# Optimization experiments

Hardware: AMD Instinct MI355X
Metric: run time of the kernel (lower is better)

Reference implementation:

```python
import jax, jax.numpy as jnp
import numpy as np

K = 8          # number of TR cores / modes
D = 1024       # categories per mode
R = 64         # TR rank
NDRAWS = 2048
EPS = 1e-30


def setup_inputs() -> dict:
    key = jax.random.key(0)
    ks = jax.random.split(key, K)
    inp = {f"log_core{i}": jax.random.normal(ks[i], (D, R, R), dtype=jnp.float32)
           for i in range(K)}
    inp["n_draws"] = NDRAWS
    return inp


def _sample(cores, n_draws, seed=1):
    """Batched version of trip_index_sample: all draws sampled in parallel."""
    k = len(cores)
    # heads[j] = S_0 @ ... @ S_{j-1} with S_i = core_i.sum(0); heads[0] = None
    heads = [None]
    acc = cores[0].sum(axis=0)
    for c in cores[1:]:
        heads.append(acc)
        acc = acc @ c.sum(axis=0)
    norm = acc  # S_0 ... S_{K-1}

    keys = jax.random.split(jax.random.key(seed), k)
    tail = None          # [B, r_{j+1}, r_K] running suffix product per draw
    idxs = []
    for step, j in enumerate(range(k - 1, -1, -1)):
        core, head = cores[j], heads[j]
        if tail is None:
            # first step (j = K-1): marginal weights shared by all draws
            if head is None:  # degenerate K == 1 case
                w = jnp.trace(core, axis1=1, axis2=2)
            else:
                w = jnp.einsum('ab,nba->n', head, core)
            ix = jax.random.categorical(keys[step], jnp.log(jnp.clip(w, EPS)),
                                        shape=(n_draws,))
            tail = core[ix]  # [B, r_j, r_K]
        else:
            # M = tail @ head : [B, r_{j+1}, r_j] (head is None only at j == 0,
            # where r_0 == r_K so tail already has the right shape)
            M = tail if head is None else tail @ head
            w = jnp.einsum('nab,Bba->Bn', core, M)  # [B, d_j]
            ix = jax.random.categorical(keys[step], jnp.log(jnp.clip(w, EPS)),
                                        axis=-1)
            tail = jnp.einsum('Bab,Bbc->Bac', core[ix], tail)
        idxs.append(ix)
    sample = jnp.stack(idxs[::-1], axis=1)  # [B, K], mode order 0..K-1
    log_p = jnp.log(jnp.clip(jnp.trace(tail, axis1=1, axis2=2), EPS)) \
            - jnp.log(jnp.trace(norm))
    return sample, log_p


def reference(log_core0, log_core1, log_core2, log_core3,
              log_core4, log_core5, log_core6, log_core7, n_draws):
    log_cores = [log_core0, log_core1, log_core2, log_core3,
                 log_core4, log_core5, log_core6, log_core7]
    cores = [jax.nn.softplus(c) for c in log_cores]
    sample, log_p = _sample(cores, n_draws)
    return sample, log_p
```

## Files before the change

kernel.cpp:

```cpp
#include <hip/hip_runtime.h>
#include <stdint.h>
#include <math.h>

#define D_CAT  1024
#define R_TR   64
#define RR     4096
#define NDRAWS 2048
#define KMODES 8

struct CorePtrs { const float* p[KMODES]; };

typedef __attribute__((ext_vector_type(8))) __bf16 bf16x8;
typedef __attribute__((ext_vector_type(4))) float  f32x4;
typedef unsigned int u32;

union BF8 { ushort u[8]; bf16x8 v; };

static __device__ inline void async_cp16(const void* g, void* l) {
  __builtin_amdgcn_global_load_lds(
      (const __attribute__((address_space(1))) u32*)g,
      (__attribute__((address_space(3))) u32*)l, 16, 0, 0);
}

static __host__ __device__ inline uint32_t rotl32(uint32_t x, int r) {
  return (x << r) | (x >> (32 - r));
}
static __host__ __device__ inline void tf2x32(uint32_t k1, uint32_t k2,
                                              uint32_t x0, uint32_t x1,
                                              uint32_t& o0, uint32_t& o1) {
  uint32_t ks0 = k1, ks1 = k2, ks2 = k1 ^ k2 ^ 0x1BD11BDAu;
  x0 += ks0; x1 += ks1;
  x0 += x1; x1 = rotl32(x1, 13); x1 ^= x0;
  x0 += x1; x1 = rotl32(x1, 15); x1 ^= x0;
  x0 += x1; x1 = rotl32(x1, 26); x1 ^= x0;
  x0 += x1; x1 = rotl32(x1, 6);  x1 ^= x0;
  x0 += ks1; x1 += ks2 + 1u;
  x0 += x1; x1 = rotl32(x1, 17); x1 ^= x0;
  x0 += x1; x1 = rotl32(x1, 29); x1 ^= x0;
  x0 += x1; x1 = rotl32(x1, 16); x1 ^= x0;
  x0 += x1; x1 = rotl32(x1, 24); x1 ^= x0;
  x0 += ks2; x1 += ks0 + 2u;
  x0 += x1; x1 = rotl32(x1, 13); x1 ^= x0;
  x0 += x1; x1 = rotl32(x1, 15); x1 ^= x0;
  x0 += x1; x1 = rotl32(x1, 26); x1 ^= x0;
  x0 += x1; x1 = rotl32(x1, 6);  x1 ^= x0;
  x0 += ks0; x1 += ks1 + 3u;
  x0 += x1; x1 = rotl32(x1, 17); x1 ^= x0;
  x0 += x1; x1 = rotl32(x1, 29); x1 ^= x0;
  x0 += x1; x1 = rotl32(x1, 16); x1 ^= x0;
  x0 += x1; x1 = rotl32(x1, 24); x1 ^= x0;
  x0 += ks1; x1 += ks2 + 4u;
  x0 += x1; x1 = rotl32(x1, 13); x1 ^= x0;
  x0 += x1; x1 = rotl32(x1, 15); x1 ^= x0;
  x0 += x1; x1 = rotl32(x1, 26); x1 ^= x0;
  x0 += x1; x1 = rotl32(x1, 6);  x1 ^= x0;
  x0 += ks2; x1 += ks0 + 5u;
  o0 = x0; o1 = x1;
}

static __device__ inline float softplus_fast(float x) {
  float e = __expf(-fabsf(x));
  return fmaxf(x, 0.0f) + __logf(1.0f + e);
}

static __device__ inline unsigned short f32_bf16(float f) {
  uint32_t u = __float_as_uint(f);
  u += 0x7fffu + ((u >> 16) & 1u);
  return (unsigned short)(u >> 16);
}

static __device__ inline float gumbel_at(uint32_t k1, uint32_t k2, uint32_t e) {
  uint32_t o0, o1;
  tf2x32(k1, k2, 0u, e, o0, o1);
  uint32_t bits = o0 ^ o1;
  float f = __uint_as_float((bits >> 9) | 0x3F800000u) - 1.0f;
  float u = (f > 0.0f) ? f : 1.17549435e-38f;
  return -logf(-logf(u));
}


__global__ void k_sentinel(float* out, int n) {
  int i = blockIdx.x * 256 + threadIdx.x;
  if (i < n) out[i] = -12288.0f;
}

__global__ __launch_bounds__(256) void k_spart(CorePtrs cp, float* __restrict__ Spart) {
  const int bid = blockIdx.x, tid = threadIdx.x;
  const int i = bid >> 8, c = bid & 255;
  const float* src = cp.p[i] + (size_t)c * 4 * RR;
  float acc[16];
#pragma unroll
  for (int k = 0; k < 16; ++k) acc[k] = 0.0f;
#pragma unroll
  for (int d = 0; d < 4; ++d) {
    const float* row = src + (size_t)d * RR;
#pragma unroll
    for (int k = 0; k < 16; ++k)
      acc[k] += softplus_fast(row[tid + k * 256]);
  }
  float* dst = Spart + (size_t)bid * RR;
#pragma unroll
  for (int k = 0; k < 16; ++k) dst[tid + k * 256] = acc[k];
}

__global__ __launch_bounds__(256) void k_sreduce(const float* __restrict__ Spart,
                                                 double* __restrict__ S) {
  const int idx = blockIdx.x * 256 + threadIdx.x;
  const int i = idx >> 12, rr = idx & 4095;
  const float* p = Spart + ((size_t)i << 20) + rr;
  double a0 = 0.0, a1 = 0.0, a2 = 0.0, a3 = 0.0;
  for (int c = 0; c < 256; c += 4) {
    a0 += (double)p[(size_t)(c + 0) * RR];
    a1 += (double)p[(size_t)(c + 1) * RR];
    a2 += (double)p[(size_t)(c + 2) * RR];
    a3 += (double)p[(size_t)(c + 3) * RR];
  }
  S[idx] = (a0 + a1) + (a2 + a3);
}

__global__ __launch_bounds__(256) void k_heads(const double* __restrict__ S,
                                               double* __restrict__ heads,
                                               double* __restrict__ misc) {
  __shared__ double cur[RR];
  __shared__ double Sm[RR];
  __shared__ double tbuf[64];
  const int tid = threadIdx.x;
  const int bcol = tid & 63;
  const int a0 = tid >> 6;
#pragma unroll
  for (int k = 0; k < 16; ++k) {
    int p = tid + k * 256;
    double v = S[p];
    cur[p] = v;
    heads[p] = v;
  }
  __syncthreads();
  for (int m = 1; m <= 6; ++m) {
#pragma unroll
    for (int k = 0; k < 16; ++k) {
      int p = tid + k * 256;
      Sm[p] = S[(size_t)m * RR + p];
    }
    __syncthreads();
    double acc[16];
#pragma unroll
    for (int k = 0; k < 16; ++k) acc[k] = 0.0;
    for (int c = 0; c < 64; ++c) {
      double s = Sm[c * 64 + bcol];
#pragma unroll
      for (int k = 0; k < 16; ++k)
        acc[k] = fma(cur[(a0 + 4 * k) * 64 + c], s, acc[k]);
    }
    __syncthreads();
#pragma unroll
    for (int k = 0; k < 16; ++k) {
      int p = tid + k * 256;
      cur[p] = acc[k];
      heads[(size_t)m * RR + p] = acc[k];
    }
    __syncthreads();
  }
#pragma unroll
  for (int k = 0; k < 16; ++k) {
    int p = tid + k * 256;
    Sm[p] = S[(size_t)7 * RR + p];
  }
  __syncthreads();
  if (tid < 64) {
    double acc = 0.0;
    for (int c = 0; c < 64; ++c)
      acc = fma(cur[tid * 64 + c], Sm[c * 64 + tid], acc);
    tbuf[tid] = acc;
  }
  __syncthreads();
  if (tid == 0) {
    double tr = 0.0;
    for (int a = 0; a < 64; ++a) tr += tbuf[a];
    misc[0] = log(tr);
  }
}

__global__ __launch_bounds__(256) void k_softplus(const float* __restrict__ src,
                                                  ushort* __restrict__ Bh,
                                                  ushort* __restrict__ Bl) {
  const size_t i4 = ((size_t)blockIdx.x * 256 + threadIdx.x) * 4;
  float4 v = *(const float4*)(src + i4);
  const float ov[4] = {softplus_fast(v.x), softplus_fast(v.y),
                       softplus_fast(v.z), softplus_fast(v.w)};
  ushort h4[4], l4[4];
#pragma unroll
  for (int q = 0; q < 4; ++q) {
    ushort h = f32_bf16(ov[q]);
    float hf = __uint_as_float((uint32_t)h << 16);
    h4[q] = h;
    l4[q] = f32_bf16(ov[q] - hf);
  }
  *(ushort4*)(Bh + i4) = make_ushort4(h4[0], h4[1], h4[2], h4[3]);
  *(ushort4*)(Bl + i4) = make_ushort4(l4[0], l4[1], l4[2], l4[3]);
}

__global__ __launch_bounds__(256) void k_w0(const float* __restrict__ raw,
                                            const double* __restrict__ head7,
                                            float* __restrict__ W) {
  const int tid = threadIdx.x;
  const int lane = tid & 63;
  const int n = blockIdx.x * 4 + (tid >> 6);
  const float* crow = raw + (size_t)n * RR;
  double acc = 0.0;
  for (int q = lane; q < RR; q += 64)
    acc = fma((double)softplus_fast(crow[q]), head7[(q & 63) * 64 + (q >> 6)], acc);
  for (int m = 32; m; m >>= 1) acc += __shfl_xor(acc, m);
  if (lane == 0) W[n] = (float)acc;
}

__global__ __launch_bounds__(256) void k_mt2(const float* __restrict__ tail,
                                             const double* __restrict__ head, int useHead,
                                             ushort* __restrict__ Ah,
                                             ushort* __restrict__ Al) {
  __shared__ alignas(16) ushort hT[2][4096];
  const int tid = threadIdx.x;
#pragma unroll
  for (int rep = 0; rep < 16; ++rep) {
    int i = tid + rep * 256;
    float v;
    if (useHead) v = (float)head[(i & 63) * 64 + (i >> 6)];
    else         v = ((i >> 6) == (i & 63)) ? 1.0f : 0.0f;
    ushort h = f32_bf16(v);
    float hf = __uint_as_float((uint32_t)h << 16);
    int dst = (i & 0xFC0) | (((((i >> 3) & 7) ^ ((i >> 6) & 7)) << 3)) | (i & 7);
    hT[0][dst] = h;
    hT[1][dst] = f32_bf16(v - hf);
  }
  __syncthreads();

  const int w = tid >> 6, l = tid & 63;
  const int B = blockIdx.x * 4 + w;
  const float* tb = tail + (size_t)B * RR;
  const int lrow = l & 15, kg = l >> 4;

  ushort* ah_out = Ah + (size_t)B * RR;
  ushort* al_out = Al + (size_t)B * RR;

  for (int it = 0; it < 4; ++it) {
    BF8 afh[2], afl[2];
#pragma unroll
    for (int kt = 0; kt < 2; ++kt) {
      const float* src = tb + (it * 16 + lrow) * 64 + kt * 32 + kg * 8;
      float4 v0 = *(const float4*)src;
      float4 v1 = *(const float4*)(src + 4);
      float vv[8] = {v0.x, v0.y, v0.z, v0.w, v1.x, v1.y, v1.z, v1.w};
#pragma unroll
      for (int q = 0; q < 8; ++q) {
        ushort h = f32_bf16(vv[q]);
        float hf = __uint_as_float((uint32_t)h << 16);
        afh[kt].u[q] = h;
        afl[kt].u[q] = f32_bf16(vv[q] - hf);
      }
    }
#pragma unroll
    for (int kt2 = 0; kt2 < 4; ++kt2) {
      f32x4 hh = (f32x4)0.0f, sm = (f32x4)0.0f;
#pragma unroll
      for (int kt = 0; kt < 2; ++kt) {
        int rowB = kt2 * 16 + lrow;
        int kcA  = kt * 4 + kg;
        int off  = rowB * 64 + ((kcA ^ (rowB & 7)) << 3);
        bf16x8 bh = *(const bf16x8*)&hT[0][off];
        bf16x8 bl = *(const bf16x8*)&hT[1][off];
        hh = __builtin_amdgcn_mfma_f32_16x16x32_bf16(afh[kt].v, bh, hh, 0, 0, 0);
        sm = __builtin_amdgcn_mfma_f32_16x16x32_bf16(afh[kt].v, bl, sm, 0, 0, 0);
        sm = __builtin_amdgcn_mfma_f32_16x16x32_bf16(afl[kt].v, bh, sm, 0, 0, 0);
      }
      ushort h4[4], l4[4];
#pragma unroll
      for (int q = 0; q < 4; ++q) {
        float v = hh[q] + sm[q];
        ushort h = f32_bf16(v);
        float hf = __uint_as_float((uint32_t)h << 16);
        h4[q] = h;
        l4[q] = f32_bf16(v - hf);
      }
      int o = (kt2 * 16 + lrow) * 64 + it * 16 + kg * 4;
      *(ushort4*)(ah_out + o) = make_ushort4(h4[0], h4[1], h4[2], h4[3]);
      *(ushort4*)(al_out + o) = make_ushort4(l4[0], l4[1], l4[2], l4[3]);
    }
  }
}

__global__ __launch_bounds__(256) void k_wgemm(const ushort* __restrict__ Ah,
                                               const ushort* __restrict__ Al,
                                               const ushort* __restrict__ Bh,
                                               const ushort* __restrict__ Bl,
                                               float* __restrict__ W) {
  __shared__ ushort lds[2][4 * 4096];
  const int tid = threadIdx.x;
  const int L = blockIdx.x;
  const int x = L & 7, j = L >> 3;
  const int bn = (x & 1) * 8 + (j & 7);
  const int bb = (x >> 1) * 8 + (j >> 3);
  const int w = tid >> 6, l = tid & 63;

  const int srow = l >> 3;
  const int skc  = l & 7;
  const ushort* gbase;
  {
    const ushort* bases[4] = {Ah + (size_t)bb * 64 * RR, Al + (size_t)bb * 64 * RR,
                              Bh + (size_t)bn * 64 * RR, Bl + (size_t)bn * 64 * RR};
    gbase = bases[w] + (size_t)srow * RR + (size_t)((skc ^ srow) * 8);
  }

  const int wm = (w >> 1) * 32, wn = (w & 1) * 32;
  const int lrow = l & 15;
  const int kg   = l >> 4;

  f32x4 acc_hh[2][2], acc_sm[2][2], hht[2][2];
#pragma unroll
  for (int mt = 0; mt < 2; ++mt)
#pragma unroll
    for (int nt = 0; nt < 2; ++nt) {
      acc_hh[mt][nt] = (f32x4)0.0f;
      acc_sm[mt][nt] = (f32x4)0.0f;
      hht[mt][nt]    = (f32x4)0.0f;
    }

  int roffA[2][2], roffB[2][2];
#pragma unroll
  for (int mt = 0; mt < 2; ++mt)
#pragma unroll
    for (int kt = 0; kt < 2; ++kt) {
      int rowA = wm + mt * 16 + lrow;
      int kcA  = kt * 4 + kg;
      roffA[mt][kt] = rowA * 64 + ((kcA ^ (rowA & 7)) << 3);
      int rowB = wn + mt * 16 + lrow;
      roffB[mt][kt] = rowB * 64 + ((kcA ^ (rowB & 7)) << 3);
    }

#pragma unroll
  for (int q = 0; q < 8; ++q)
    async_cp16(gbase + (size_t)q * 8 * RR, &lds[0][w * 4096 + q * 512]);

  for (int t = 0; t < 64; ++t) {
    const int bf = t & 1;
    __syncthreads();
    if (t < 63) {
      const int koff = (t + 1) * 64;
#pragma unroll
      for (int q = 0; q < 8; ++q)
        async_cp16(gbase + (size_t)q * 8 * RR + koff,
                   &lds[bf ^ 1][w * 4096 + q * 512]);
    }
    const ushort* L2 = lds[bf];
#pragma unroll
    for (int kt = 0; kt < 2; ++kt) {
      bf16x8 ah[2], al[2], bh[2], bl[2];
#pragma unroll
      for (int mt = 0; mt < 2; ++mt) {
        ah[mt] = *(const bf16x8*)&L2[0 * 4096 + roffA[mt][kt]];
        al[mt] = *(const bf16x8*)&L2[1 * 4096 + roffA[mt][kt]];
      }
#pragma unroll
      for (int nt = 0; nt < 2; ++nt) {
        bh[nt] = *(const bf16x8*)&L2[2 * 4096 + roffB[nt][kt]];
        bl[nt] = *(const bf16x8*)&L2[3 * 4096 + roffB[nt][kt]];
      }
#pragma unroll
      for (int mt = 0; mt < 2; ++mt)
#pragma unroll
        for (int nt = 0; nt < 2; ++nt) {
          acc_hh[mt][nt] = __builtin_amdgcn_mfma_f32_16x16x32_bf16(ah[mt], bh[nt], acc_hh[mt][nt], 0, 0, 0);
          acc_sm[mt][nt] = __builtin_amdgcn_mfma_f32_16x16x32_bf16(ah[mt], bl[nt], acc_sm[mt][nt], 0, 0, 0);
          acc_sm[mt][nt] = __builtin_amdgcn_mfma_f32_16x16x32_bf16(al[mt], bh[nt], acc_sm[mt][nt], 0, 0, 0);
        }
    }
    if ((t & 15) == 15) {
#pragma unroll
      for (int mt = 0; mt < 2; ++mt)
#pragma unroll
        for (int nt = 0; nt < 2; ++nt) {
          hht[mt][nt] += acc_hh[mt][nt];
          acc_hh[mt][nt] = (f32x4)0.0f;
        }
    }
  }

#pragma unroll
  for (int mt = 0; mt < 2; ++mt)
#pragma unroll
    for (int nt = 0; nt < 2; ++nt)
#pragma unroll
      for (int q = 0; q < 4; ++q) {
        int gr = bb * 64 + wm + mt * 16 + kg * 4 + q;
        int gc = bn * 64 + wn + nt * 16 + lrow;
        W[(size_t)gr * D_CAT + gc] = hht[mt][nt][q] + acc_sm[mt][nt][q];
      }
}

__global__ __launch_bounds__(256) void k_sample(const float* __restrict__ W, int shared_row,
                                                uint32_t key1, uint32_t key2,
                                                int* __restrict__ ixout,
                                                float* __restrict__ out, int mode_j) {
  const int b = blockIdx.x, tid = threadIdx.x;
  const float* wrow = W + (shared_row ? 0 : (size_t)b * D_CAT);
  float best = -3.4e38f; int bidx = 0x7fffffff;
  for (int k = 0; k < 4; ++k) {
    int n = tid + k * 256;
    float lg = logf(fmaxf(wrow[n], 1e-30f));
    float v = gumbel_at(key1, key2, (uint32_t)(b * D_CAT + n)) + lg;
    if (v > best || (v == best && n < bidx)) { best = v; bidx = n; }
  }
  for (int m = 32; m; m >>= 1) {
    float ov = __shfl_xor(best, m);
    int   oi = __shfl_xor(bidx, m);
    if (ov > best || (ov == best && oi < bidx)) { best = ov; bidx = oi; }
  }
  __shared__ float sv[4];
  __shared__ int   si[4];
  if ((tid & 63) == 0) { sv[tid >> 6] = best; si[tid >> 6] = bidx; }
  __syncthreads();
  if (tid == 0) {
    for (int t = 1; t < 4; ++t)
      if (sv[t] > best || (sv[t] == best && si[t] < bidx)) { best = sv[t]; bidx = si[t]; }
    ixout[b] = bidx;
    out[b * KMODES + mode_j] = (float)bidx;
  }
}

__global__ __launch_bounds__(256) void k_tail2(const float* __restrict__ raw,
                                               const ushort* __restrict__ Bh,
                                               const ushort* __restrict__ Bl,
                                               const int* __restrict__ ix,
                                               float* __restrict__ tail, int first) {
  const int B = blockIdx.x;
  const int tid = threadIdx.x;
  const int m = ix[B];
  float* trow = tail + (size_t)B * RR;
  if (first) {
    const float* crow = raw + (size_t)m * RR;
#pragma unroll
    for (int r = 0; r < 4; ++r) {
      float4 v = *(const float4*)(crow + tid * 4 + r * 1024);
      float4 o;
      o.x = softplus_fast(v.x); o.y = softplus_fast(v.y);
      o.z = softplus_fast(v.z); o.w = softplus_fast(v.w);
      *(float4*)(trow + tid * 4 + r * 1024) = o;
    }
    return;
  }
  __shared__ alignas(16) ushort Th[4096];
  __shared__ alignas(16) ushort Tl[4096];
  const ushort* ch = Bh + (size_t)m * RR;
  const ushort* cl = Bl + (size_t)m * RR;

#pragma unroll
  for (int r = 0; r < 4; ++r) {
    int p = tid * 4 + r * 1024;
    int i = p >> 6, k = p & 63;
    float4 v = *(const float4*)(trow + p);
    float vv[4] = {v.x, v.y, v.z, v.w};
#pragma unroll
    for (int q = 0; q < 4; ++q) {
      int row = k + q;
      int dst = row * 64 + ((((i >> 3) ^ (row & 7)) << 3)) + (i & 7);
      ushort h = f32_bf16(vv[q]);
      float hf = __uint_as_float((uint32_t)h << 16);
      Th[dst] = h;
      Tl[dst] = f32_bf16(vv[q] - hf);
    }
  }
  __syncthreads();

  const int w = tid >> 6, l = tid & 63;
  const int lrow = l & 15, kg = l >> 4;
  bf16x8 ah[2], al[2];
#pragma unroll
  for (int kt = 0; kt < 2; ++kt) {
    int off = (w * 16 + lrow) * 64 + kt * 32 + kg * 8;
    ah[kt] = *(const bf16x8*)(ch + off);
    al[kt] = *(const bf16x8*)(cl + off);
  }
#pragma unroll
  for (int jt = 0; jt < 4; ++jt) {
    f32x4 hh = (f32x4)0.0f, sm = (f32x4)0.0f;
#pragma unroll
    for (int kt = 0; kt < 2; ++kt) {
      int rowB = jt * 16 + lrow;
      int kcA  = kt * 4 + kg;
      int off  = rowB * 64 + ((kcA ^ (rowB & 7)) << 3);
      bf16x8 bh = *(const bf16x8*)&Th[off];
      bf16x8 bl = *(const bf16x8*)&Tl[off];
      hh = __builtin_amdgcn_mfma_f32_16x16x32_bf16(ah[kt], bh, hh, 0, 0, 0);
      sm = __builtin_amdgcn_mfma_f32_16x16x32_bf16(ah[kt], bl, sm, 0, 0, 0);
      sm = __builtin_amdgcn_mfma_f32_16x16x32_bf16(al[kt], bh, sm, 0, 0, 0);
      sm = __builtin_amdgcn_mfma_f32_16x16x32_bf16(al[kt], bl, sm, 0, 0, 0);
    }
#pragma unroll
    for (int q = 0; q < 4; ++q)
      trow[(w * 16 + kg * 4 + q) * 64 + jt * 16 + lrow] = hh[q] + sm[q];
  }
}

__global__ __launch_bounds__(256) void k_logp(const float* __restrict__ tail,
                                              const double* __restrict__ misc,
                                              float* __restrict__ out) {
  const int b = blockIdx.x * 256 + threadIdx.x;
  double tr = 0.0;
  for (int a = 0; a < 64; ++a) tr += (double)tail[(size_t)b * RR + a * 65];
  double lp = log(fmax(tr, 1e-30)) - misc[0];
  out[NDRAWS * KMODES + b] = (float)lp;
}

extern "C" void kernel_launch(void* const* d_in, const int* in_sizes, int n_in,
                              void* d_out, int out_size, void* d_ws, size_t ws_size,
                              hipStream_t stream) {
  (void)in_sizes; (void)n_in;
  CorePtrs cp;
  for (int i = 0; i < KMODES; ++i) cp.p[i] = (const float*)d_in[i];
  float* outf = (float*)d_out;

  char* base = (char*)d_ws;
  const size_t o_w     = 0;
  const size_t o_tail  = o_w + (size_t)NDRAWS * D_CAT * 4;
  const size_t o_ahl   = o_tail + (size_t)NDRAWS * RR * 4;
  const size_t o_spart = o_ahl;
  const size_t o_S     = o_ahl + (size_t)NDRAWS * RR * 4;
  const size_t o_heads = o_S + (size_t)KMODES * RR * 8;
  const size_t o_ix    = o_heads + (size_t)7 * RR * 8;
  const size_t o_misc  = o_ix + (size_t)NDRAWS * 4;
  const size_t o_bh    = o_misc + 256;
  const size_t o_bl    = o_bh + (size_t)D_CAT * RR * 2;
  const size_t NEED    = o_bl + (size_t)D_CAT * RR * 2;
  if (ws_size < NEED) {
    k_sentinel<<<(out_size + 255) / 256, 256, 0, stream>>>(outf, out_size);
    return;
  }

  float*  W     = (float*)(base + o_w);
  float*  tail  = (float*)(base + o_tail);
  ushort* Ah    = (ushort*)(base + o_ahl);
  ushort* Al    = Ah + (size_t)NDRAWS * RR;
  float*  Spart = (float*)(base + o_spart);
  double* S     = (double*)(base + o_S);
  double* heads = (double*)(base + o_heads);
  int*    ix    = (int*)(base + o_ix);
  double* misc  = (double*)(base + o_misc);
  ushort* Bh    = (ushort*)(base + o_bh);
  ushort* Bl    = (ushort*)(base + o_bl);

  uint32_t kk1[KMODES], kk2[KMODES];
  for (uint32_t s = 0; s < KMODES; ++s) tf2x32(0u, 1u, 0u, s, kk1[s], kk2[s]);

  k_spart  <<<2048, 256, 0, stream>>>(cp, Spart);
  k_sreduce<<<128,  256, 0, stream>>>(Spart, S);
  k_heads  <<<1,    256, 0, stream>>>(S, heads, misc);

  for (int s = 0; s < KMODES; ++s) {
    const int j = 7 - s;
    if (s == 0) {
      k_w0<<<256, 256, 0, stream>>>(cp.p[7], heads + (size_t)6 * RR, W);
    } else {
      k_softplus<<<4096, 256, 0, stream>>>(cp.p[j], Bh, Bl);
      k_mt2<<<512, 256, 0, stream>>>(tail, j > 0 ? heads + (size_t)(j - 1) * RR : nullptr,
                                     j > 0 ? 1 : 0, Ah, Al);
      k_wgemm<<<512, 256, 0, stream>>>(Ah, Al, Bh, Bl, W);
    }
    k_sample<<<NDRAWS, 256, 0, stream>>>(W, s == 0 ? 1 : 0, kk1[s], kk2[s], ix, outf, j);
    k_tail2 <<<2048, 256, 0, stream>>>(cp.p[j], Bh, Bl, ix, tail, s == 0 ? 1 : 0);
  }
  k_logp<<<KMODES, 256, 0, stream>>>(tail, misc, outf);
}
```

Measured before the change: 905.9 us.

## Fuse softplus with tail-head product and sampling with tail update kernels

Merges the per-mode softplus/bf16 split and the tail@head transform into one launch, with block ranges selecting the role. Merges categorical sampling with the tail update so the sampled index stays in shared memory instead of going through a global ix buffer. For the last mode (no head), replaces the identity-matrix MFMA product with a plain LDS transpose and bf16 split. This removes several kernel launches per mode and some redundant work. The cost is larger shared memory per block in the fused sampling kernel, which may lower occupancy.

```diff
diff --git a/kernel.cpp b/kernel.cpp
--- a/kernel.cpp
+++ b/kernel.cpp
@@ -180,25 +180,6 @@
   }
 }
 
-__global__ __launch_bounds__(256) void k_softplus(const float* __restrict__ src,
-                                                  ushort* __restrict__ Bh,
-                                                  ushort* __restrict__ Bl) {
-  const size_t i4 = ((size_t)blockIdx.x * 256 + threadIdx.x) * 4;
-  float4 v = *(const float4*)(src + i4);
-  const float ov[4] = {softplus_fast(v.x), softplus_fast(v.y),
-                       softplus_fast(v.z), softplus_fast(v.w)};
-  ushort h4[4], l4[4];
-#pragma unroll
-  for (int q = 0; q < 4; ++q) {
-    ushort h = f32_bf16(ov[q]);
-    float hf = __uint_as_float((uint32_t)h << 16);
-    h4[q] = h;
-    l4[q] = f32_bf16(ov[q] - hf);
-  }
-  *(ushort4*)(Bh + i4) = make_ushort4(h4[0], h4[1], h4[2], h4[3]);
-  *(ushort4*)(Bl + i4) = make_ushort4(l4[0], l4[1], l4[2], l4[3]);
-}
-
 __global__ __launch_bounds__(256) void k_w0(const float* __restrict__ raw,
                                             const double* __restrict__ head7,
                                             float* __restrict__ W) {
@@ -213,76 +194,129 @@
   if (lane == 0) W[n] = (float)acc;
 }
 
-__global__ __launch_bounds__(256) void k_mt2(const float* __restrict__ tail,
-                                             const double* __restrict__ head, int useHead,
-                                             ushort* __restrict__ Ah,
-                                             ushort* __restrict__ Al) {
-  __shared__ alignas(16) ushort hT[2][4096];
-  const int tid = threadIdx.x;
-#pragma unroll
-  for (int rep = 0; rep < 16; ++rep) {
-    int i = tid + rep * 256;
-    float v;
-    if (useHead) v = (float)head[(i & 63) * 64 + (i >> 6)];
-    else         v = ((i >> 6) == (i & 63)) ? 1.0f : 0.0f;
-    ushort h = f32_bf16(v);
-    float hf = __uint_as_float((uint32_t)h << 16);
-    int dst = (i & 0xFC0) | (((((i >> 3) & 7) ^ ((i >> 6) & 7)) << 3)) | (i & 7);
-    hT[0][dst] = h;
-    hT[1][dst] = f32_bf16(v - hf);
-  }
-  __syncthreads();
-
-  const int w = tid >> 6, l = tid & 63;
-  const int B = blockIdx.x * 4 + w;
-  const float* tb = tail + (size_t)B * RR;
-  const int lrow = l & 15, kg = l >> 4;
-
-  ushort* ah_out = Ah + (size_t)B * RR;
-  ushort* al_out = Al + (size_t)B * RR;
-
-  for (int it = 0; it < 4; ++it) {
-    BF8 afh[2], afl[2];
-#pragma unroll
-    for (int kt = 0; kt < 2; ++kt) {
-      const float* src = tb + (it * 16 + lrow) * 64 + kt * 32 + kg * 8;
-      float4 v0 = *(const float4*)src;
-      float4 v1 = *(const float4*)(src + 4);
-      float vv[8] = {v0.x, v0.y, v0.z, v0.w, v1.x, v1.y, v1.z, v1.w};
-#pragma unroll
-      for (int q = 0; q < 8; ++q) {
-        ushort h = f32_bf16(vv[q]);
-        float hf = __uint_as_float((uint32_t)h << 16);
-        afh[kt].u[q] = h;
-        afl[kt].u[q] = f32_bf16(vv[q] - hf);
+__global__ __launch_bounds__(256) void k_spmt(const float* __restrict__ src,
+                                              ushort* __restrict__ Bh,
+                                              ushort* __restrict__ Bl,
+                                              const float* __restrict__ tail,
+                                              const double* __restrict__ head, int useHead,
+                                              ushort* __restrict__ Ah,
+                                              ushort* __restrict__ Al) {
+  __shared__ alignas(16) float smem[4176];
+  const int bid = blockIdx.x, tid = threadIdx.x;
+  if (bid < 4096) {
+    const size_t i4 = ((size_t)bid * 256 + tid) * 4;
+    float4 v = *(const float4*)(src + i4);
+    const float ov[4] = {softplus_fast(v.x), softplus_fast(v.y),
+                         softplus_fast(v.z), softplus_fast(v.w)};
+    ushort h4[4], l4[4];
+#pragma unroll
+    for (int q = 0; q < 4; ++q) {
+      ushort h = f32_bf16(ov[q]);
+      float hf = __uint_as_float((uint32_t)h << 16);
+      h4[q] = h;
+      l4[q] = f32_bf16(ov[q] - hf);
+    }
+    *(ushort4*)(Bh + i4) = make_ushort4(h4[0], h4[1], h4[2], h4[3]);
+    *(ushort4*)(Bl + i4) = make_ushort4(l4[0], l4[1], l4[2], l4[3]);
+    return;
+  }
+  const int blk = bid - 4096;
+  if (useHead) {
+    ushort (*hT)[4096] = (ushort(*)[4096])smem;
+#pragma unroll
+    for (int rep = 0; rep < 16; ++rep) {
+      int i = tid + rep * 256;
+      float v = (float)head[(i & 63) * 64 + (i >> 6)];
+      ushort h = f32_bf16(v);
+      float hf = __uint_as_float((uint32_t)h << 16);
+      int dst = (i & 0xFC0) | (((((i >> 3) & 7) ^ ((i >> 6) & 7)) << 3)) | (i & 7);
+      hT[0][dst] = h;
+      hT[1][dst] = f32_bf16(v - hf);
+    }
+    __syncthreads();
+    const int w = tid >> 6, l = tid & 63;
+    const int B = blk * 4 + w;
+    const float* tb = tail + (size_t)B * RR;
+    const int lrow = l & 15, kg = l >> 4;
+    ushort* ah_out = Ah + (size_t)B * RR;
+    ushort* al_out = Al + (size_t)B * RR;
+    for (int it = 0; it < 4; ++it) {
+      BF8 afh[2], afl[2];
+#pragma unroll
+      for (int kt = 0; kt < 2; ++kt) {
+        const float* s2 = tb + (it * 16 + lrow) * 64 + kt * 32 + kg * 8;
+        float4 v0 = *(const float4*)s2;
+        float4 v1 = *(const float4*)(s2 + 4);
+        float vv[8] = {v0.x, v0.y, v0.z, v0.w, v1.x, v1.y, v1.z, v1.w};
+#pragma unroll
+        for (int q = 0; q < 8; ++q) {
+          ushort h = f32_bf16(vv[q]);
+          float hf = __uint_as_float((uint32_t)h << 16);
+          afh[kt].u[q] = h;
+          afl[kt].u[q] = f32_bf16(vv[q] - hf);
+        }
       }
-    }
-#pragma unroll
-    for (int kt2 = 0; kt2 < 4; ++kt2) {
-      f32x4 hh = (f32x4)0.0f, sm = (f32x4)0.0f;
-#pragma unroll
-      for (int kt = 0; kt < 2; ++kt) {
-        int rowB = kt2 * 16 + lrow;
-        int kcA  = kt * 4 + kg;
-        int off  = rowB * 64 + ((kcA ^ (rowB & 7)) << 3);
-        bf16x8 bh = *(const bf16x8*)&hT[0][off];
-        bf16x8 bl = *(const bf16x8*)&hT[1][off];
-        hh = __builtin_amdgcn_mfma_f32_16x16x32_bf16(afh[kt].v, bh, hh, 0, 0, 0);
-        sm = __builtin_amdgcn_mfma_f32_16x16x32_bf16(afh[kt].v, bl, sm, 0, 0, 0);
-        sm = __builtin_amdgcn_mfma_f32_16x16x32_bf16(afl[kt].v, bh, sm, 0, 0, 0);
+#pragma unroll
+      for (int kt2 = 0; kt2 < 4; ++kt2) {
+        f32x4 hh = (f32x4)0.0f, sm = (f32x4)0.0f;
+#pragma unroll
+        for (int kt = 0; kt < 2; ++kt) {
+          int rowB = kt2 * 16 + lrow;
+          int kcA  = kt * 4 + kg;
+          int off  = rowB * 64 + ((kcA ^ (rowB & 7)) << 3);
+          bf16x8 bh = *(const bf16x8*)&hT[0][off];
+          bf16x8 bl = *(const bf16x8*)&hT[1][off];
+          hh = __builtin_amdgcn_mfma_f32_16x16x32_bf16(afh[kt].v, bh, hh, 0, 0, 0);
+          sm = __builtin_amdgcn_mfma_f32_16x16x32_bf16(afh[kt].v, bl, sm, 0, 0, 0);
+          sm = __builtin_amdgcn_mfma_f32_16x16x32_bf16(afl[kt].v, bh, sm, 0, 0, 0);
+        }
+        ushort h4[4], l4[4];
+#pragma unroll
+        for (int q = 0; q < 4; ++q) {
+          float v = hh[q] + sm[q];
+          ushort h = f32_bf16(v);
+          float hf = __uint_as_float((uint32_t)h << 16);
+          h4[q] = h;
+          l4[q] = f32_bf16(v - hf);
+        }
+        int o = (kt2 * 16 + lrow) * 64 + it * 16 + kg * 4;
+        *(ushort4*)(ah_out + o) = make_ushort4(h4[0], h4[1], h4[2], h4[3]);
+        *(ushort4*)(al_out + o) = make_ushort4(l4[0], l4[1], l4[2], l4[3]);
       }
-      ushort h4[4], l4[4];
-#pragma unroll
-      for (int q = 0; q < 4; ++q) {
-        float v = hh[q] + sm[q];
-        ushort h = f32_bf16(v);
-        float hf = __uint_as_float((uint32_t)h << 16);
-        h4[q] = h;
-        l4[q] = f32_bf16(v - hf);
+    }
+  } else {
+    float* tl = smem;
+    for (int d = 0; d < 4; ++d) {
+      const int B = blk * 4 + d;
+      const float* tb = tail + (size_t)B * RR;
+      ushort* ah_out = Ah + (size_t)B * RR;
+      ushort* al_out = Al + (size_t)B * RR;
+      __syncthreads();
+#pragma unroll
+      for (int r = 0; r < 4; ++r) {
+        int p = tid * 4 + r * 1024;
+        int i = p >> 6, k = p & 63;
+        float4 v = *(const float4*)(tb + p);
+        tl[i * 65 + k + 0] = v.x; tl[i * 65 + k + 1] = v.y;
+        tl[i * 65 + k + 2] = v.z; tl[i * 65 + k + 3] = v.w;
       }
-      int o = (kt2 * 16 + lrow) * 64 + it * 16 + kg * 4;
-      *(ushort4*)(ah_out + o) = make_ushort4(h4[0], h4[1], h4[2], h4[3]);
-      *(ushort4*)(al_out + o) = make_ushort4(l4[0], l4[1], l4[2], l4[3]);
+      __syncthreads();
+#pragma unroll
+      for (int r = 0; r < 4; ++r) {
+        int p = tid * 4 + r * 1024;
+        int k = p >> 6, i0 = p & 63;
+        ushort h4[4], l4[4];
+#pragma unroll
+        for (int q = 0; q < 4; ++q) {
+          float m = tl[(i0 + q) * 65 + k];
+          ushort h = f32_bf16(m);
+          float hf = __uint_as_float((uint32_t)h << 16);
+          h4[q] = h;
+          l4[q] = f32_bf16(m - hf);
+        }
+        *(ushort4*)(ah_out + p) = make_ushort4(h4[0], h4[1], h4[2], h4[3]);
+        *(ushort4*)(al_out + p) = make_ushort4(l4[0], l4[1], l4[2], l4[3]);
+      }
     }
   }
 }
@@ -395,45 +429,47 @@
       }
 }
 
-__global__ __launch_bounds__(256) void k_sample(const float* __restrict__ W, int shared_row,
-                                                uint32_t key1, uint32_t key2,
-                                                int* __restrict__ ixout,
-                                                float* __restrict__ out, int mode_j) {
-  const int b = blockIdx.x, tid = threadIdx.x;
-  const float* wrow = W + (shared_row ? 0 : (size_t)b * D_CAT);
-  float best = -3.4e38f; int bidx = 0x7fffffff;
-  for (int k = 0; k < 4; ++k) {
-    int n = tid + k * 256;
-    float lg = logf(fmaxf(wrow[n], 1e-30f));
-    float v = gumbel_at(key1, key2, (uint32_t)(b * D_CAT + n)) + lg;
-    if (v > best || (v == best && n < bidx)) { best = v; bidx = n; }
-  }
-  for (int m = 32; m; m >>= 1) {
-    float ov = __shfl_xor(best, m);
-    int   oi = __shfl_xor(bidx, m);
-    if (ov > best || (ov == best && oi < bidx)) { best = ov; bidx = oi; }
-  }
+__global__ __launch_bounds__(256) void k_samptail(const float* __restrict__ W, int shared_row,
+                                                  uint32_t key1, uint32_t key2,
+                                                  float* __restrict__ out, int mode_j,
+                                                  const float* __restrict__ raw,
+                                                  const ushort* __restrict__ Bh,
+                                                  const ushort* __restrict__ Bl,
+                                                  float* __restrict__ tail, int first) {
   __shared__ float sv[4];
   __shared__ int   si[4];
-  if ((tid & 63) == 0) { sv[tid >> 6] = best; si[tid >> 6] = bidx; }
-  __syncthreads();
-  if (tid == 0) {
-    for (int t = 1; t < 4; ++t)
-      if (sv[t] > best || (sv[t] == best && si[t] < bidx)) { best = sv[t]; bidx = si[t]; }
-    ixout[b] = bidx;
-    out[b * KMODES + mode_j] = (float)bidx;
-  }
-}
-
-__global__ __launch_bounds__(256) void k_tail2(const float* __restrict__ raw,
-                                               const ushort* __restrict__ Bh,
-                                               const ushort* __restrict__ Bl,
-                                               const int* __restrict__ ix,
-                                               float* __restrict__ tail, int first) {
-  const int B = blockIdx.x;
-  const int tid = threadIdx.x;
-  const int m = ix[B];
-  float* trow = tail + (size_t)B * RR;
+  __shared__ int   s_m;
+  __shared__ alignas(16) ushort Th[4096];
+  __shared__ alignas(16) ushort Tl[4096];
+  const int b = blockIdx.x, tid = threadIdx.x;
+
+  {
+    const float* wrow = W + (shared_row ? 0 : (size_t)b * D_CAT);
+    float best = -3.4e38f; int bidx = 0x7fffffff;
+    for (int k = 0; k < 4; ++k) {
+      int n = tid + k * 256;
+      float lg = logf(fmaxf(wrow[n], 1e-30f));
+      float v = gumbel_at(key1, key2, (uint32_t)(b * D_CAT + n)) + lg;
+      if (v > best || (v == best && n < bidx)) { best = v; bidx = n; }
+    }
+    for (int m = 32; m; m >>= 1) {
+      float ov = __shfl_xor(best, m);
+      int   oi = __shfl_xor(bidx, m);
+      if (ov > best || (ov == best && oi < bidx)) { best = ov; bidx = oi; }
+    }
+    if ((tid & 63) == 0) { sv[tid >> 6] = best; si[tid >> 6] = bidx; }
+    __syncthreads();
+    if (tid == 0) {
+      for (int t = 1; t < 4; ++t)
+        if (sv[t] > best || (sv[t] == best && si[t] < bidx)) { best = sv[t]; bidx = si[t]; }
+      s_m = bidx;
+      out[b * KMODES + mode_j] = (float)bidx;
+    }
+    __syncthreads();
+  }
+  const int m = s_m;
+  float* trow = tail + (size_t)b * RR;
+
   if (first) {
     const float* crow = raw + (size_t)m * RR;
 #pragma unroll
@@ -446,8 +482,6 @@
     }
     return;
   }
-  __shared__ alignas(16) ushort Th[4096];
-  __shared__ alignas(16) ushort Tl[4096];
   const ushort* ch = Bh + (size_t)m * RR;
   const ushort* cl = Bl + (size_t)m * RR;
 
@@ -524,8 +558,7 @@
   const size_t o_spart = o_ahl;
   const size_t o_S     = o_ahl + (size_t)NDRAWS * RR * 4;
   const size_t o_heads = o_S + (size_t)KMODES * RR * 8;
-  const size_t o_ix    = o_heads + (size_t)7 * RR * 8;
-  const size_t o_misc  = o_ix + (size_t)NDRAWS * 4;
+  const size_t o_misc  = o_heads + (size_t)7 * RR * 8;
   const size_t o_bh    = o_misc + 256;
   const size_t o_bl    = o_bh + (size_t)D_CAT * RR * 2;
   const size_t NEED    = o_bl + (size_t)D_CAT * RR * 2;
@@ -541,7 +574,6 @@
   float*  Spart = (float*)(base + o_spart);
   double* S     = (double*)(base + o_S);
   double* heads = (double*)(base + o_heads);
-  int*    ix    = (int*)(base + o_ix);
   double* misc  = (double*)(base + o_misc);
   ushort* Bh    = (ushort*)(base + o_bh);
   ushort* Bl    = (ushort*)(base + o_bl);
@@ -558,13 +590,14 @@
     if (s == 0) {
       k_w0<<<256, 256, 0, stream>>>(cp.p[7], heads + (size_t)6 * RR, W);
     } else {
-      k_softplus<<<4096, 256, 0, stream>>>(cp.p[j], Bh, Bl);
-      k_mt2<<<512, 256, 0, stream>>>(tail, j > 0 ? heads + (size_t)(j - 1) * RR : nullptr,
-                                     j > 0 ? 1 : 0, Ah, Al);
+      k_spmt<<<4608, 256, 0, stream>>>(cp.p[j], Bh, Bl, tail,
+                                       j > 0 ? heads + (size_t)(j - 1) * RR : heads,
+                                       j > 0 ? 1 : 0, Ah, Al);
       k_wgemm<<<512, 256, 0, stream>>>(Ah, Al, Bh, Bl, W);
     }
-    k_sample<<<NDRAWS, 256, 0, stream>>>(W, s == 0 ? 1 : 0, kk1[s], kk2[s], ix, outf, j);
-    k_tail2 <<<2048, 256, 0, stream>>>(cp.p[j], Bh, Bl, ix, tail, s == 0 ? 1 : 0);
+    k_samptail<<<NDRAWS, 256, 0, stream>>>(W, s == 0 ? 1 : 0, kk1[s], kk2[s],
+                                           outf, j, cp.p[j], Bh, Bl, tail,
+                                           s == 0 ? 1 : 0);
   }
   k_logp<<<KMODES, 256, 0, stream>>>(tail, misc, outf);
 }
```

New measurement: 866.8 us. 4.3% less time.
